# Kernel optimization log

Hardware: AMD Instinct MI355X
Metric: run time of the kernel (lower is better)

## Reference

```python
import jax, jax.numpy as jnp
import numpy as np

B, N, C, H = 16, 1024, 768, 12
D = C // H
SCALE = D ** -0.5


def setup_inputs() -> dict:
    key = jax.random.key(0)
    k1, k2, k3, k4, k5 = jax.random.split(key, 5)
    return {
        "x": jax.random.normal(k1, (B, N, C), dtype=jnp.float32),
        "qkv_w": jax.random.normal(k2, (3 * C, C), dtype=jnp.float32) * (C ** -0.5),
        "qkv_b": jax.random.normal(k3, (3 * C,), dtype=jnp.float32) * 0.02,
        "proj_w": jax.random.normal(k4, (C, C), dtype=jnp.float32) * (C ** -0.5),
        "proj_b": jax.random.normal(k5, (C,), dtype=jnp.float32) * 0.02,
    }


def reference(x, qkv_w, qkv_b, proj_w, proj_b):
    # x: [B, N, C]. torch Linear: y = x @ W.T + b
    b, n, c = x.shape
    qkv = x @ qkv_w.T + qkv_b                      # [B, N, 3C]
    qkv = qkv.reshape(b, n, 3, H, D).transpose(2, 0, 3, 1, 4)  # [3, B, H, N, D]
    q, k, v = qkv[0], qkv[1], qkv[2]
    # dropout is identity in eval mode; scores scaled by head_dim**-0.5
    scores = jnp.einsum("bhnd,bhmd->bhnm", q, k) * SCALE  # [B, H, N, N]
    attn = jax.nn.softmax(scores, axis=-1)
    out = jnp.einsum("bhnm,bhmd->bhnd", attn, v)           # [B, H, N, D]
    out = out.transpose(0, 2, 1, 3).reshape(b, n, c)       # [B, N, C]
    return out @ proj_w.T + proj_b
```

## Files before the change

### kernel.cpp

```cpp
#include <hip/hip_runtime.h>
#include <hip/hip_bf16.h>


typedef __attribute__((ext_vector_type(8))) short short8;
typedef __attribute__((ext_vector_type(4))) float floatx4;

constexpr int Bsz = 16, Nseq = 1024, Cdim = 768, Hh = 12, Dd = 64;
constexpr float SCALE = 0.125f;

__device__ __forceinline__ ushort f2bs(float f) {
    union { __hip_bfloat16 h; ushort u; } cv;
    cv.h = __float2bfloat16(f);
    return cv.u;
}
__device__ __forceinline__ void stF(float* p, float v) { *p = v; }
__device__ __forceinline__ void stF(ushort* p, float v) { *p = f2bs(v); }

__device__ __forceinline__ void gld16(void* lds, const void* g) {
    __builtin_amdgcn_global_load_lds(
        (const __attribute__((address_space(1))) unsigned int*)g,
        (__attribute__((address_space(3))) unsigned int*)lds, 16, 0, 0);
}

__global__ __launch_bounds__(256) void pack_bf16(
        const float* __restrict__ x, const float* __restrict__ w1,
        const float* __restrict__ w2, ushort* __restrict__ xb,
        ushort* __restrict__ w1b, ushort* __restrict__ w2b) {
    const size_t n0 = (size_t)Bsz * Nseq * Cdim;
    const size_t n1 = (size_t)3 * Cdim * Cdim;
    size_t i = ((size_t)blockIdx.x * 256 + threadIdx.x) * 4;
    const float* src;
    ushort* dst;
    if (i < n0) { src = x; dst = xb; }
    else if (i < n0 + n1) { i -= n0; src = w1; dst = w1b; }
    else { i -= n0 + n1; src = w2; dst = w2b; }
    float4 v = *(const float4*)&src[i];
    *(ushort4*)&dst[i] = make_ushort4(f2bs(v.x), f2bs(v.y), f2bs(v.z), f2bs(v.w));
}

template <typename TO>
__global__ __launch_bounds__(256) void gemm_nt_mfma(
        const ushort* __restrict__ A, const ushort* __restrict__ Bw,
        const float* __restrict__ bias, TO* __restrict__ C0,
        ushort* __restrict__ vt, int split, int ld0,
        int M, int N, int K, int vmode) {
    __shared__ ushort As[128 * 64];
    __shared__ ushort Bs[128 * 64];
    const int t = threadIdx.x;
    const int lane = t & 63;
    const int w = t >> 6;
    const int quad = lane >> 4;
    const int l16 = lane & 15;
    const int m0 = blockIdx.y * 128;
    const int n0 = blockIdx.x * 128;
    const int mw = (w >> 1) * 64;
    const int nw = (w & 1) * 64;
    const int srow = lane >> 3;
    const int schunk = lane & 7;

    floatx4 acc[4][4];
#pragma unroll
    for (int i = 0; i < 4; ++i)
#pragma unroll
        for (int j = 0; j < 4; ++j) acc[i][j] = (floatx4)0.0f;

    for (int k0 = 0; k0 < K; k0 += 64) {
        __syncthreads();
#pragma unroll
        for (int i = 0; i < 4; ++i) {
            int r0 = (w * 4 + i) * 8;
            int row = r0 + srow;
            int cs = (schunk ^ (row & 7)) * 8;
            gld16(&As[r0 * 64], &A[(size_t)(m0 + row) * K + k0 + cs]);
            gld16(&Bs[r0 * 64], &Bw[(size_t)(n0 + row) * K + k0 + cs]);
        }
        __syncthreads();

#pragma unroll
        for (int kk = 0; kk < 2; ++kk) {
            const int pc = ((kk * 4 + quad) ^ (l16 & 7)) * 8;
            short8 af[4], bfr[4];
#pragma unroll
            for (int i = 0; i < 4; ++i)
                af[i] = *(const short8*)&As[(mw + i * 16 + l16) * 64 + pc];
#pragma unroll
            for (int j = 0; j < 4; ++j)
                bfr[j] = *(const short8*)&Bs[(nw + j * 16 + l16) * 64 + pc];
#pragma unroll
            for (int i = 0; i < 4; ++i)
#pragma unroll
                for (int j = 0; j < 4; ++j)
                    acc[i][j] = __builtin_amdgcn_mfma_f32_16x16x32_bf16(
                        af[i], bfr[j], acc[i][j], 0, 0, 0);
        }
    }

#pragma unroll
    for (int j = 0; j < 4; ++j) {
        int col = n0 + nw + j * 16 + l16;
        float bc = bias[col];
        if (vmode && col >= split) {
            int ch = col - split;
            int h = ch >> 6, d = ch & 63;
#pragma unroll
            for (int i = 0; i < 4; ++i)
#pragma unroll
                for (int r = 0; r < 4; ++r) {
                    int row = m0 + mw + i * 16 + quad * 4 + r;
                    int b = row >> 10, n = row & 1023;
                    vt[(((size_t)(b * Hh + h)) * Dd + d) * Nseq + n] =
                        f2bs(acc[i][j][r] + bc);
                }
        } else {
#pragma unroll
            for (int i = 0; i < 4; ++i)
#pragma unroll
                for (int r = 0; r < 4; ++r) {
                    int row = m0 + mw + i * 16 + quad * 4 + r;
                    stF(&C0[(size_t)row * ld0 + col], acc[i][j][r] + bc);
                }
        }
    }
}

__global__ __launch_bounds__(256) void attn_mfma(const ushort* __restrict__ qk,
                                                 const ushort* __restrict__ vt,
                                                 ushort* __restrict__ outp) {
    __shared__ ushort Ks[64 * 64];
    __shared__ ushort Vts[64 * 64];
    __shared__ ushort Ps[4][32][72];

    const int t = threadIdx.x;
    const int lane = t & 63;
    const int w = t >> 6;
    const int quad = lane >> 4;
    const int l16 = lane & 15;
    const int srow = lane >> 3;
    const int schunk = lane & 7;

    const int bid = blockIdx.x;
    const int qt = bid & 7;
    const int bh = bid >> 3;
    const int h = bh % Hh, b = bh / Hh;

    const size_t rs = 2 * Cdim;
    const ushort* qbase = qk + (size_t)b * Nseq * rs + h * Dd;
    const ushort* kbase = qbase + Cdim;
    const ushort* vbase = vt + (size_t)bh * Dd * Nseq;

    short8 aq[2][2];
#pragma unroll
    for (int mt = 0; mt < 2; ++mt)
#pragma unroll
        for (int kc = 0; kc < 2; ++kc) {
            int q = qt * 128 + w * 32 + mt * 16 + l16;
            aq[mt][kc] = *(const short8*)&qbase[(size_t)q * rs + kc * 32 + quad * 8];
        }

    floatx4 o[2][4];
    float lsum[2][4];
#pragma unroll
    for (int mt = 0; mt < 2; ++mt) {
#pragma unroll
        for (int dt = 0; dt < 4; ++dt) o[mt][dt] = (floatx4)0.0f;
#pragma unroll
        for (int r = 0; r < 4; ++r) lsum[mt][r] = 0.f;
    }

    for (int kt = 0; kt < Nseq; kt += 64) {
        __syncthreads();
#pragma unroll
        for (int i = 0; i < 2; ++i) {
            int r0 = (w * 2 + i) * 8;
            int row = r0 + srow;
            int cs = (schunk ^ (row & 7)) * 8;
            gld16(&Ks[r0 * 64], &kbase[(size_t)(kt + row) * rs + cs]);
            gld16(&Vts[r0 * 64], &vbase[(size_t)row * Nseq + kt + cs]);
        }
        __syncthreads();

        floatx4 s[2][4];
#pragma unroll
        for (int mt = 0; mt < 2; ++mt)
#pragma unroll
            for (int nt = 0; nt < 4; ++nt) s[mt][nt] = (floatx4)0.0f;
#pragma unroll
        for (int kc = 0; kc < 2; ++kc) {
            const int pc = ((kc * 4 + quad) ^ (l16 & 7)) * 8;
            short8 bk[4];
#pragma unroll
            for (int nt = 0; nt < 4; ++nt)
                bk[nt] = *(const short8*)&Ks[(nt * 16 + l16) * 64 + pc];
#pragma unroll
            for (int mt = 0; mt < 2; ++mt)
#pragma unroll
                for (int nt = 0; nt < 4; ++nt)
                    s[mt][nt] = __builtin_amdgcn_mfma_f32_16x16x32_bf16(
                        aq[mt][kc], bk[nt], s[mt][nt], 0, 0, 0);
        }

#pragma unroll
        for (int mt = 0; mt < 2; ++mt)
#pragma unroll
            for (int nt = 0; nt < 4; ++nt)
#pragma unroll
                for (int r = 0; r < 4; ++r) {
                    float p = __expf(s[mt][nt][r] * SCALE);
                    lsum[mt][r] += p;
                    Ps[w][mt * 16 + quad * 4 + r][nt * 16 + l16] = f2bs(p);
                }

#pragma unroll
        for (int kc = 0; kc < 2; ++kc) {
            const int pcv = ((kc * 4 + quad) ^ (l16 & 7)) * 8;
            short8 ap[2];
#pragma unroll
            for (int mt = 0; mt < 2; ++mt)
                ap[mt] = *(const short8*)&Ps[w][mt * 16 + l16][kc * 32 + quad * 8];
#pragma unroll
            for (int dt = 0; dt < 4; ++dt) {
                short8 bv = *(const short8*)&Vts[(dt * 16 + l16) * 64 + pcv];
#pragma unroll
                for (int mt = 0; mt < 2; ++mt)
                    o[mt][dt] = __builtin_amdgcn_mfma_f32_16x16x32_bf16(
                        ap[mt], bv, o[mt][dt], 0, 0, 0);
            }
        }
    }

#pragma unroll
    for (int mt = 0; mt < 2; ++mt)
#pragma unroll
        for (int r = 0; r < 4; ++r) {
            float v = lsum[mt][r];
            v += __shfl_xor(v, 1);
            v += __shfl_xor(v, 2);
            v += __shfl_xor(v, 4);
            v += __shfl_xor(v, 8);
            lsum[mt][r] = v;
        }
#pragma unroll
    for (int mt = 0; mt < 2; ++mt)
#pragma unroll
        for (int dt = 0; dt < 4; ++dt)
#pragma unroll
            for (int r = 0; r < 4; ++r) {
                int q = qt * 128 + w * 32 + mt * 16 + quad * 4 + r;
                int d = dt * 16 + l16;
                outp[((size_t)(b * Nseq + q)) * Cdim + h * Dd + d] =
                    f2bs(o[mt][dt][r] / lsum[mt][r]);
            }
}

extern "C" void kernel_launch(void* const* d_in, const int* in_sizes, int n_in,
                              void* d_out, int out_size, void* d_ws, size_t ws_size,
                              hipStream_t stream) {
    const float* x      = (const float*)d_in[0];
    const float* qkv_w  = (const float*)d_in[1];
    const float* qkv_b  = (const float*)d_in[2];
    const float* proj_w = (const float*)d_in[3];
    const float* proj_b = (const float*)d_in[4];
    float* out = (float*)d_out;

    const int M = Bsz * Nseq;
    ushort* xb    = (ushort*)d_ws;
    ushort* qk    = xb + (size_t)M * Cdim;
    ushort* vtbuf = qk + (size_t)M * 2 * Cdim;
    ushort* wqkvb = vtbuf + (size_t)Hh * Bsz * Dd * Nseq;
    ushort* wprjb = wqkvb + (size_t)3 * Cdim * Cdim;
    ushort* attnout = xb;

    pack_bf16<<<14592, 256, 0, stream>>>(x, qkv_w, proj_w, xb, wqkvb, wprjb);
    gemm_nt_mfma<ushort><<<dim3(18, 128), 256, 0, stream>>>(
        xb, wqkvb, qkv_b, qk, vtbuf, 2 * Cdim, 2 * Cdim, M, 3 * Cdim, Cdim, 1);
    attn_mfma<<<Bsz * Hh * (Nseq / 128), 256, 0, stream>>>(qk, vtbuf, attnout);
    gemm_nt_mfma<float><<<dim3(6, 128), 256, 0, stream>>>(
        attnout, wprjb, proj_b, out, vtbuf, 1 << 30, Cdim, M, Cdim, Cdim, 0);
}
```

Baseline: 311.9 us.

## Double-buffer K/V tiles in attention, transpose S layout, fold scale into Q GEMM

```diff
diff --git a/kernel.cpp b/kernel.cpp
--- a/kernel.cpp
+++ b/kernel.cpp
@@ -43,7 +43,7 @@
         const ushort* __restrict__ A, const ushort* __restrict__ Bw,
         const float* __restrict__ bias, TO* __restrict__ C0,
         ushort* __restrict__ vt, int split, int ld0,
-        int M, int N, int K, int vmode) {
+        int M, int N, int K, int vmode, int qsplit, float qscale) {
     __shared__ ushort As[128 * 64];
     __shared__ ushort Bs[128 * 64];
     const int t = threadIdx.x;
@@ -99,6 +99,7 @@
     for (int j = 0; j < 4; ++j) {
         int col = n0 + nw + j * 16 + l16;
         float bc = bias[col];
+        float sc = (col < qsplit) ? qscale : 1.0f;
         if (vmode && col >= split) {
             int ch = col - split;
             int h = ch >> 6, d = ch & 63;
@@ -117,7 +118,7 @@
 #pragma unroll
                 for (int r = 0; r < 4; ++r) {
                     int row = m0 + mw + i * 16 + quad * 4 + r;
-                    stF(&C0[(size_t)row * ld0 + col], acc[i][j][r] + bc);
+                    stF(&C0[(size_t)row * ld0 + col], (acc[i][j][r] + bc) * sc);
                 }
         }
     }
@@ -126,8 +127,8 @@
 __global__ __launch_bounds__(256) void attn_mfma(const ushort* __restrict__ qk,
                                                  const ushort* __restrict__ vt,
                                                  ushort* __restrict__ outp) {
-    __shared__ ushort Ks[64 * 64];
-    __shared__ ushort Vts[64 * 64];
+    __shared__ ushort Ks[2][64 * 64];
+    __shared__ ushort Vts[2][64 * 64];
     __shared__ ushort Ps[4][32][72];
 
     const int t = threadIdx.x;
@@ -139,8 +140,8 @@
     const int schunk = lane & 7;
 
     const int bid = blockIdx.x;
-    const int qt = bid & 7;
-    const int bh = bid >> 3;
+    const int qt = (bid >> 3) & 7;
+    const int bh = (bid & 7) + 8 * (bid >> 6);
     const int h = bh % Hh, b = bh / Hh;
 
     const size_t rs = 2 * Cdim;
@@ -150,65 +151,72 @@
 
     short8 aq[2][2];
 #pragma unroll
-    for (int mt = 0; mt < 2; ++mt)
+    for (int qn = 0; qn < 2; ++qn)
 #pragma unroll
         for (int kc = 0; kc < 2; ++kc) {
-            int q = qt * 128 + w * 32 + mt * 16 + l16;
-            aq[mt][kc] = *(const short8*)&qbase[(size_t)q * rs + kc * 32 + quad * 8];
-        }
-
-    floatx4 o[2][4];
-    float lsum[2][4];
-#pragma unroll
-    for (int mt = 0; mt < 2; ++mt) {
-#pragma unroll
-        for (int dt = 0; dt < 4; ++dt) o[mt][dt] = (floatx4)0.0f;
-#pragma unroll
-        for (int r = 0; r < 4; ++r) lsum[mt][r] = 0.f;
-    }
-
-    for (int kt = 0; kt < Nseq; kt += 64) {
-        __syncthreads();
+            int q = qt * 128 + w * 32 + qn * 16 + l16;
+            aq[qn][kc] = *(const short8*)&qbase[(size_t)q * rs + kc * 32 + quad * 8];
+        }
+
+    auto stage = [&](int kt64, int buf) {
 #pragma unroll
         for (int i = 0; i < 2; ++i) {
             int r0 = (w * 2 + i) * 8;
             int row = r0 + srow;
             int cs = (schunk ^ (row & 7)) * 8;
-            gld16(&Ks[r0 * 64], &kbase[(size_t)(kt + row) * rs + cs]);
-            gld16(&Vts[r0 * 64], &vbase[(size_t)row * Nseq + kt + cs]);
-        }
+            gld16(&Ks[buf][r0 * 64], &kbase[(size_t)(kt64 * 64 + row) * rs + cs]);
+            gld16(&Vts[buf][r0 * 64], &vbase[(size_t)row * Nseq + kt64 * 64 + cs]);
+        }
+    };
+
+    floatx4 o[2][4];
+    float lsum[2] = {0.f, 0.f};
+#pragma unroll
+    for (int mt = 0; mt < 2; ++mt)
+#pragma unroll
+        for (int dt = 0; dt < 4; ++dt) o[mt][dt] = (floatx4)0.0f;
+
+    stage(0, 0);
+    for (int kt = 0; kt < Nseq / 64; ++kt) {
         __syncthreads();
-
-        floatx4 s[2][4];
-#pragma unroll
-        for (int mt = 0; mt < 2; ++mt)
-#pragma unroll
-            for (int nt = 0; nt < 4; ++nt) s[mt][nt] = (floatx4)0.0f;
+        if (kt + 1 < Nseq / 64) stage(kt + 1, (kt + 1) & 1);
+        const ushort* Kb = Ks[kt & 1];
+        const ushort* Vb = Vts[kt & 1];
+
+        floatx4 st[4][2];
+#pragma unroll
+        for (int km = 0; km < 4; ++km)
+#pragma unroll
+            for (int qn = 0; qn < 2; ++qn) st[km][qn] = (floatx4)0.0f;
 #pragma unroll
         for (int kc = 0; kc < 2; ++kc) {
             const int pc = ((kc * 4 + quad) ^ (l16 & 7)) * 8;
-            short8 bk[4];
-#pragma unroll
-            for (int nt = 0; nt < 4; ++nt)
-                bk[nt] = *(const short8*)&Ks[(nt * 16 + l16) * 64 + pc];
-#pragma unroll
-            for (int mt = 0; mt < 2; ++mt)
-#pragma unroll
-                for (int nt = 0; nt < 4; ++nt)
-                    s[mt][nt] = __builtin_amdgcn_mfma_f32_16x16x32_bf16(
-                        aq[mt][kc], bk[nt], s[mt][nt], 0, 0, 0);
-        }
-
-#pragma unroll
-        for (int mt = 0; mt < 2; ++mt)
-#pragma unroll
-            for (int nt = 0; nt < 4; ++nt)
-#pragma unroll
-                for (int r = 0; r < 4; ++r) {
-                    float p = __expf(s[mt][nt][r] * SCALE);
-                    lsum[mt][r] += p;
-                    Ps[w][mt * 16 + quad * 4 + r][nt * 16 + l16] = f2bs(p);
-                }
+            short8 ak[4];
+#pragma unroll
+            for (int km = 0; km < 4; ++km)
+                ak[km] = *(const short8*)&Kb[(km * 16 + l16) * 64 + pc];
+#pragma unroll
+            for (int km = 0; km < 4; ++km)
+#pragma unroll
+                for (int qn = 0; qn < 2; ++qn)
+                    st[km][qn] = __builtin_amdgcn_mfma_f32_16x16x32_bf16(
+                        ak[km], aq[qn][kc], st[km][qn], 0, 0, 0);
+        }
+
+#pragma unroll
+        for (int km = 0; km < 4; ++km)
+#pragma unroll
+            for (int qn = 0; qn < 2; ++qn) {
+                float p0 = __expf(st[km][qn][0]);
+                float p1 = __expf(st[km][qn][1]);
+                float p2 = __expf(st[km][qn][2]);
+                float p3 = __expf(st[km][qn][3]);
+                lsum[qn] += (p0 + p1) + (p2 + p3);
+                uint2 pk;
+                pk.x = (uint)f2bs(p0) | ((uint)f2bs(p1) << 16);
+                pk.y = (uint)f2bs(p2) | ((uint)f2bs(p3) << 16);
+                *(uint2*)&Ps[w][qn * 16 + l16][km * 16 + quad * 4] = pk;
+            }
 
 #pragma unroll
         for (int kc = 0; kc < 2; ++kc) {
@@ -219,7 +227,7 @@
                 ap[mt] = *(const short8*)&Ps[w][mt * 16 + l16][kc * 32 + quad * 8];
 #pragma unroll
             for (int dt = 0; dt < 4; ++dt) {
-                short8 bv = *(const short8*)&Vts[(dt * 16 + l16) * 64 + pcv];
+                short8 bv = *(const short8*)&Vb[(dt * 16 + l16) * 64 + pcv];
 #pragma unroll
                 for (int mt = 0; mt < 2; ++mt)
                     o[mt][dt] = __builtin_amdgcn_mfma_f32_16x16x32_bf16(
@@ -229,26 +237,23 @@
     }
 
 #pragma unroll
+    for (int qn = 0; qn < 2; ++qn) {
+        float v = lsum[qn];
+        v += __shfl_xor(v, 16);
+        v += __shfl_xor(v, 32);
+        lsum[qn] = v;
+    }
+#pragma unroll
     for (int mt = 0; mt < 2; ++mt)
 #pragma unroll
-        for (int r = 0; r < 4; ++r) {
-            float v = lsum[mt][r];
-            v += __shfl_xor(v, 1);
-            v += __shfl_xor(v, 2);
-            v += __shfl_xor(v, 4);
-            v += __shfl_xor(v, 8);
-            lsum[mt][r] = v;
-        }
-#pragma unroll
-    for (int mt = 0; mt < 2; ++mt)
-#pragma unroll
         for (int dt = 0; dt < 4; ++dt)
 #pragma unroll
             for (int r = 0; r < 4; ++r) {
+                float li = __shfl(lsum[mt], quad * 4 + r);
                 int q = qt * 128 + w * 32 + mt * 16 + quad * 4 + r;
                 int d = dt * 16 + l16;
                 outp[((size_t)(b * Nseq + q)) * Cdim + h * Dd + d] =
-                    f2bs(o[mt][dt][r] / lsum[mt][r]);
+                    f2bs(o[mt][dt][r] / li);
             }
 }
 
@@ -272,8 +277,10 @@
 
     pack_bf16<<<14592, 256, 0, stream>>>(x, qkv_w, proj_w, xb, wqkvb, wprjb);
     gemm_nt_mfma<ushort><<<dim3(18, 128), 256, 0, stream>>>(
-        xb, wqkvb, qkv_b, qk, vtbuf, 2 * Cdim, 2 * Cdim, M, 3 * Cdim, Cdim, 1);
+        xb, wqkvb, qkv_b, qk, vtbuf, 2 * Cdim, 2 * Cdim, M, 3 * Cdim, Cdim, 1,
+        Cdim, SCALE);
     attn_mfma<<<Bsz * Hh * (Nseq / 128), 256, 0, stream>>>(qk, vtbuf, attnout);
     gemm_nt_mfma<float><<<dim3(6, 128), 256, 0, stream>>>(
-        attnout, wprjb, proj_b, out, vtbuf, 1 << 30, Cdim, M, Cdim, Cdim, 0);
-}
+        attnout, wprjb, proj_b, out, vtbuf, 1 << 30, Cdim, M, Cdim, Cdim, 0,
+        0, 1.0f);
+}
```

New measurement: 296.9 us. 1.05x faster.
